# Optimization experiments

Hardware: AMD Instinct MI355X
Metric: run time of the kernel (lower is better)

The kernel has to match this reference:

```python
import jax, jax.numpy as jnp
import numpy as np

B, T, N, H, DH = 32, 64, 100, 4, 32  # batch, seq, nodes, heads, dim/head


def setup_inputs() -> dict:
    key = jax.random.key(0)
    ks = jax.random.split(key, 20)
    # structured flat observation: [action_mask(132), adj(100*100), dt(1), obs(256), siem(128)]
    am = (jax.random.uniform(ks[0], (B, T, 132)) < 0.8).astype(jnp.float32)
    adj = (jax.random.uniform(ks[1], (B, T, N * N)) < 0.05).astype(jnp.float32)
    dt = jax.random.uniform(ks[2], (B, T, 1)) * 0.1 + 0.01
    obs = jax.random.normal(ks[3], (B, T, 256))
    siem = jax.random.normal(ks[4], (B, T, 128))
    inputs = jnp.concatenate([am, adj, dt, obs, siem], axis=-1)
    s = 0.05
    return dict(
        inputs=inputs,
        h0=jnp.zeros((B, 128), jnp.float32),
        fc_w=jax.random.normal(ks[5], (384, 256)) * s,
        fc_b=jnp.zeros((256,)),
        gat_w=jax.random.normal(ks[6], (256, H, DH)) * s,
        a_src=jax.random.normal(ks[7], (H, DH)) * s,
        a_dst=jax.random.normal(ks[8], (H, DH)) * s,
        ode_w1=jax.random.normal(ks[9], (128, 128)) * s,
        ode_b1=jnp.zeros((128,)),
        ode_w2=jax.random.normal(ks[10], (128, 128)) * s,
        ode_b2=jnp.zeros((128,)),
        gru_wi=jax.random.normal(ks[11], (128, 384)) * s,
        gru_wh=jax.random.normal(ks[12], (128, 384)) * s,
        gru_bi=jnp.zeros((384,)),
        gru_bh=jnp.zeros((384,)),
        act_w=jax.random.normal(ks[13], (128, 132)) * s,
        act_b=jnp.zeros((132,)),
        val_w=jax.random.normal(ks[14], (128, 1)) * s,
        val_b=jnp.zeros((1,)),
    )


def reference(inputs, h0, fc_w, fc_b, gat_w, a_src, a_dst, ode_w1, ode_b1,
              ode_w2, ode_b2, gru_wi, gru_wh, gru_bi, gru_bh, act_w, act_b,
              val_w, val_b):
    Bt, Tt = inputs.shape[0], inputs.shape[1]
    action_mask = inputs[..., :132]
    adj_raw = inputs[..., 132:10132].reshape(Bt * Tt, N, N)
    dtn = inputs[..., 10132:10133]                      # [B,T,1]
    x = jnp.concatenate([inputs[..., 10133:10389], inputs[..., 10389:10517]], -1)
    x = jax.nn.relu(x @ fc_w + fc_b).reshape(Bt * Tt, 256)
    # SubnetMaskGenerator.create_mask: binary adjacency + self loops
    adj = (adj_raw > 0) | jnp.eye(N, dtype=bool)[None]
    # place per-agent embedding at node 0, rest zero
    x_nodes = jnp.zeros((Bt * Tt, N, 256), x.dtype).at[:, 0, :].set(x)
    Wh = jnp.einsum('bnf,fhd->bhnd', x_nodes, gat_w)
    src = jnp.einsum('bhnd,hd->bhn', Wh, a_src)
    dst = jnp.einsum('bhnd,hd->bhn', Wh, a_dst)
    e = jax.nn.leaky_relu(src[:, :, :, None] + dst[:, :, None, :], 0.2)
    e = jnp.where(adj[:, None, :, :], e, -1e9)
    alpha = jax.nn.softmax(e, axis=-1)
    hgat = jax.nn.elu(jnp.einsum('bhij,bhjd->bhid', alpha, Wh))
    hgat = hgat.transpose(0, 2, 1, 3).reshape(Bt * Tt, N, H * DH)
    x_gat = hgat.mean(axis=1).reshape(Bt, Tt, 128)

    def f(h):  # ODE dynamics net
        return jnp.tanh(jnp.tanh(h @ ode_w1 + ode_b1) @ ode_w2 + ode_b2)

    def step(h, inp):
        xt, dt = inp                                    # [B,128], [B,1]
        k1 = f(h)
        k2 = f(h + 0.5 * dt * k1)
        k3 = f(h + 0.5 * dt * k2)
        k4 = f(h + dt * k3)
        h_ode = h + dt / 6.0 * (k1 + 2 * k2 + 2 * k3 + k4)
        gi = xt @ gru_wi + gru_bi
        gh = h_ode @ gru_wh + gru_bh
        ir, iz, inn = jnp.split(gi, 3, -1)
        hr, hz, hn = jnp.split(gh, 3, -1)
        r = jax.nn.sigmoid(ir + hr)
        z = jax.nn.sigmoid(iz + hz)
        n = jnp.tanh(inn + r * hn)
        h_new = (1.0 - z) * n + z * h_ode
        return h_new, h_new

    h_T, hs = jax.lax.scan(step, h0, (x_gat.transpose(1, 0, 2), dtn.transpose(1, 0, 2)))
    x_rnn = hs.transpose(1, 0, 2)                       # [B,T,128]
    logits = x_rnn @ act_w + act_b
    value = (x_rnn @ val_w + val_b).reshape(-1)
    masked_logits = jnp.where(action_mask == 0.0, jnp.float32(-1e10), logits)
    return masked_logits, h_T, value
```

## Files before the change

### kernel.cpp

```cpp
#include <hip/hip_runtime.h>

#define NIN 10517
typedef unsigned short ushort_t;
using f32x4  = __attribute__((ext_vector_type(4))) float;
using bf16x8 = __attribute__((ext_vector_type(8))) short;

__device__ __forceinline__ float lrelu02(float x){ return x > 0.f ? x : 0.2f*x; }
__device__ __forceinline__ float fast_tanh(float x){ float e=__expf(2.f*x); return 1.f - 2.f/(e+1.f); }
__device__ __forceinline__ float fast_sig(float x){ return 1.f/(1.f+__expf(-x)); }

__device__ __forceinline__ ushort_t f2bf(float x){
  unsigned u = __float_as_uint(x);
  unsigned r = u + 0x7FFF + ((u >> 16) & 1);
  return (ushort_t)(r >> 16);
}
__device__ __forceinline__ float bf2f(ushort_t v){ return __uint_as_float(((unsigned)v) << 16); }

#define LBAR() do { asm volatile("s_waitcnt lgkmcnt(0)" ::: "memory"); \
                    __builtin_amdgcn_s_barrier(); } while (0)

__global__ __launch_bounds__(256) void k_fc_gat(const float* __restrict__ inputs,
    const float* __restrict__ fc_w, const float* __restrict__ fc_b,
    const float* __restrict__ gat_w, const float* __restrict__ a_src, const float* __restrict__ a_dst,
    const float* __restrict__ ode_w1, const float* __restrict__ ode_w2, const float* __restrict__ gru_wh,
    const float* __restrict__ act_w,
    float* __restrict__ wh0_ws, float* __restrict__ sd_ws,
    ushort_t* __restrict__ w1B, ushort_t* __restrict__ w2B, ushort_t* __restrict__ ghB,
    ushort_t* __restrict__ actB)
{
  __shared__ float xin[8][384];
  __shared__ float xfc[8][256];
  __shared__ float wh[8][128];
  const int tid = threadIdx.x;
  const int bt0 = blockIdx.x * 8;

  for (int p = blockIdx.x * 256 + tid; p < 100352; p += 256*256) {
    if (p < 49152) {
      int m = p >> 7, k = p & 127;
      ghB[p] = f2bf(gru_wh[k*384 + m]);
    } else if (p < 65536) {
      int q = p - 49152, jj = q >> 7, k = q & 127;
      w1B[q] = f2bf(ode_w1[k*128 + jj]);
    } else if (p < 81920) {
      int q = p - 65536, jj = q >> 7, k = q & 127;
      w2B[q] = f2bf(ode_w2[k*128 + jj]);
    } else {
      int q = p - 81920, col = q >> 7, k = q & 127;
      actB[q] = (col < 132) ? f2bf(act_w[k*132 + col]) : (ushort_t)0;
    }
  }

  for (int idx = tid; idx < 8*384; idx += 256) {
    int r = idx / 384, f = idx - r*384;
    xin[r][f] = inputs[(size_t)(bt0+r)*NIN + 10133 + f];
  }
  __syncthreads();
  {
    float acc[8];
    float bj = fc_b[tid];
    #pragma unroll
    for (int r=0;r<8;r++) acc[r] = bj;
    for (int f=0; f<384; f++) {
      float wf = fc_w[f*256 + tid];
      #pragma unroll
      for (int r=0;r<8;r++) acc[r] = fmaf(xin[r][f], wf, acc[r]);
    }
    #pragma unroll
    for (int r=0;r<8;r++) xfc[r][tid] = fmaxf(acc[r], 0.f);
  }
  __syncthreads();
  {
    const int j2 = tid & 127, r0 = (tid >> 7) * 4;
    float acc[4];
    #pragma unroll
    for (int r=0;r<4;r++) acc[r] = 0.f;
    for (int f=0; f<256; f++) {
      float wf = gat_w[f*128 + j2];
      #pragma unroll
      for (int r=0;r<4;r++) acc[r] = fmaf(xfc[r0+r][f], wf, acc[r]);
    }
    #pragma unroll
    for (int r=0;r<4;r++) {
      wh[r0+r][j2] = acc[r];
      wh0_ws[(size_t)(bt0+r0+r)*128 + j2] = acc[r];
    }
  }
  __syncthreads();
  if (tid < 64) {
    const int r = tid >> 3, h = (tid >> 1) & 3, w = tid & 1;
    const float* av = w ? a_dst : a_src;
    float acc = 0.f;
    #pragma unroll
    for (int d=0; d<32; d++) acc = fmaf(wh[r][h*32+d], av[h*32+d], acc);
    sd_ws[(size_t)(bt0+r)*8 + w*4 + h] = acc;
  }
}

__global__ __launch_bounds__(256) void k_alpha_gi(const float* __restrict__ inputs,
    const float* __restrict__ wh0_ws, const float* __restrict__ sd_ws,
    const float* __restrict__ gru_wi, const float* __restrict__ gru_bi,
    float* __restrict__ gi_ws)
{
  __shared__ int cnt[100];
  __shared__ int a0f[100];
  __shared__ float alpha[4][100];
  __shared__ float wh0[128];
  __shared__ float sdl[8];
  __shared__ float xg[128];
  __shared__ float psum[256];
  const int tid = threadIdx.x;
  const size_t bt = blockIdx.x;
  if (tid < 128) wh0[tid] = wh0_ws[bt*128 + tid];
  if (tid < 8) sdl[tid] = sd_ws[bt*8 + tid];
  const float* adj = inputs + bt*NIN + 132;
  const int wv = tid >> 6, lane = tid & 63;
  for (int i = wv; i < 100; i += 4) {
    float v0 = adj[i*100 + lane];
    int pred0 = (lane != 0) && ((v0 > 0.f) || (lane == i));
    unsigned long long b0 = __ballot(pred0);
    int pred1 = 0;
    if (lane < 36) {
      float v1 = adj[i*100 + 64 + lane];
      pred1 = (v1 > 0.f) || ((64 + lane) == i);
    }
    unsigned long long b1 = __ballot(pred1);
    if (lane == 0) {
      cnt[i] = __popcll(b0) + __popcll(b1);
      a0f[i] = (v0 > 0.f) ? 1 : 0;
    }
  }
  __syncthreads();
  for (int idx = tid; idx < 400; idx += 256) {
    int h = idx / 100, i = idx - h*100;
    float s = sdl[h], d = sdl[4+h];
    float a;
    if (i == 0) {
      float ea = __expf(lrelu02(s + d));
      float eb = __expf(lrelu02(s));
      a = ea / (ea + (float)cnt[0] * eb);
    } else if (a0f[i]) {
      float ed = __expf(lrelu02(d));
      a = ed / (ed + (float)cnt[i]);
    } else {
      a = 0.f;
    }
    alpha[h][i] = a;
  }
  __syncthreads();
  {
    const int pr = tid & 127, hf = tid >> 7;
    const float w = wh0[pr];
    const int hh = pr >> 5;
    float sum = 0.f;
    const int i0 = hf * 50;
    for (int i = i0; i < i0 + 50; i++) {
      float t = alpha[hh][i] * w;
      sum += (t > 0.f) ? t : (__expf(t) - 1.f);
    }
    psum[tid] = sum;
  }
  __syncthreads();
  if (tid < 128) xg[tid] = (psum[tid] + psum[tid+128]) * 0.01f;
  __syncthreads();
  for (int jj = tid; jj < 384; jj += 256) {
    float acc = gru_bi[jj];
    for (int f=0; f<128; f++) acc = fmaf(xg[f], gru_wi[f*384 + jj], acc);
    gi_ws[bt*384 + jj] = acc;
  }
}

__global__ __launch_bounds__(512) void k_rnn(const float* __restrict__ inputs,
    const float* __restrict__ h0,
    const ushort_t* __restrict__ w1B, const float* __restrict__ ode_b1,
    const ushort_t* __restrict__ w2B, const float* __restrict__ ode_b2,
    const ushort_t* __restrict__ ghB, const float* __restrict__ gru_bh,
    const ushort_t* __restrict__ actB, const float* __restrict__ act_b,
    const float* __restrict__ val_w, const float* __restrict__ val_b,
    const float* __restrict__ gi_ws,
    float* __restrict__ out_logits, float* __restrict__ out_hT, float* __restrict__ out_val)
{
  __shared__ __align__(16) ushort_t bufA[128];
  __shared__ __align__(16) ushort_t bufB[128];
  __shared__ __align__(16) ushort_t bufC[128];
  __shared__ float dtbuf[64];
  __shared__ __align__(16) ushort_t hsbuf[64*136];
  const int tid = threadIdx.x;
  const int b = blockIdx.x;
  const int w = tid >> 6, lane = tid & 63;
  const int li = lane & 15, g = lane >> 4;
  const int col = w*16 + li;

  bf16x8 W1f[4], W2f[4], GAf[4], GBf[4], GCf[4];
  #pragma unroll
  for (int kt=0;kt<4;kt++){
    const int o = kt*32 + g*8;
    W1f[kt] = *reinterpret_cast<const bf16x8*>(w1B + col*128 + o);
    W2f[kt] = *reinterpret_cast<const bf16x8*>(w2B + col*128 + o);
    GAf[kt] = *reinterpret_cast<const bf16x8*>(ghB + (size_t)col*128       + o);
    GBf[kt] = *reinterpret_cast<const bf16x8*>(ghB + (size_t)(col+128)*128 + o);
    GCf[kt] = *reinterpret_cast<const bf16x8*>(ghB + (size_t)(col+256)*128 + o);
  }
  const float b1 = ode_b1[col], b2 = ode_b2[col];
  const float bh0 = gru_bh[col], bh1 = gru_bh[col+128], bh2 = gru_bh[col+256];
  float h = h0[b*128 + col];
  if (tid < 64) dtbuf[tid] = inputs[((size_t)b*64 + tid)*NIN + 10132];
  if (lane < 16) bufC[col] = f2bf(h);
  const float* gib = gi_ws + (size_t)b*64*384 + col;
  __syncthreads();

  bf16x8 af[4];
  auto ldaf = [&](const ushort_t* __restrict__ hb){
    #pragma unroll
    for (int kt=0;kt<4;kt++) af[kt] = *reinterpret_cast<const bf16x8*>(hb + kt*32 + g*8);
  };
  auto mvac = [&](const bf16x8 (&Wf)[4])->float{
    const f32x4 z0 = {0.f,0.f,0.f,0.f};
    f32x4 c0 = __builtin_amdgcn_mfma_f32_16x16x32_bf16(af[0], Wf[0], z0, 0,0,0);
    f32x4 c1 = __builtin_amdgcn_mfma_f32_16x16x32_bf16(af[1], Wf[1], z0, 0,0,0);
    f32x4 c2 = __builtin_amdgcn_mfma_f32_16x16x32_bf16(af[2], Wf[2], z0, 0,0,0);
    f32x4 c3 = __builtin_amdgcn_mfma_f32_16x16x32_bf16(af[3], Wf[3], z0, 0,0,0);
    return (c0[0]+c1[0]) + (c2[0]+c3[0]);
  };

  for (int t=0; t<64; t++) {
    const float dt = dtbuf[t];
    const float gir = gib[(size_t)t*384];
    const float giz = gib[(size_t)t*384 + 128];
    const float gin = gib[(size_t)t*384 + 256];

    float u, k1, k2, k3, k4;
    ldaf(bufC); u  = fast_tanh(mvac(W1f)+b1); if (lane<16) bufA[col]=f2bf(u);                    LBAR();
    ldaf(bufA); k1 = fast_tanh(mvac(W2f)+b2); if (lane<16) bufB[col]=f2bf(fmaf(0.5f*dt,k1,h));   LBAR();
    ldaf(bufB); u  = fast_tanh(mvac(W1f)+b1); if (lane<16) bufA[col]=f2bf(u);                    LBAR();
    ldaf(bufA); k2 = fast_tanh(mvac(W2f)+b2); if (lane<16) bufB[col]=f2bf(fmaf(0.5f*dt,k2,h));   LBAR();
    ldaf(bufB); u  = fast_tanh(mvac(W1f)+b1); if (lane<16) bufA[col]=f2bf(u);                    LBAR();
    ldaf(bufA); k3 = fast_tanh(mvac(W2f)+b2); if (lane<16) bufB[col]=f2bf(fmaf(dt,k3,h));        LBAR();
    ldaf(bufB); u  = fast_tanh(mvac(W1f)+b1); if (lane<16) bufA[col]=f2bf(u);                    LBAR();
    ldaf(bufA); k4 = fast_tanh(mvac(W2f)+b2);
    const float h_ode = fmaf(dt*(1.f/6.f), (k1 + 2.f*k2) + (2.f*k3 + k4), h);
    if (lane<16) bufB[col] = f2bf(h_ode);                                                        LBAR();

    ldaf(bufB);
    {
      const float r = fast_sig(gir + mvac(GAf) + bh0);
      const float z = fast_sig(giz + mvac(GBf) + bh1);
      const float n = fast_tanh(gin + r*(mvac(GCf) + bh2));
      h = (1.f - z)*n + z*h_ode;
    }
    if (lane < 16) {
      bufC[col] = f2bf(h);
      hsbuf[t*136 + col] = f2bf(h);
    }
    LBAR();
  }

  if (lane < 16) out_hT[b*128 + col] = h;

  {
    const int rt = w & 3, ch = w >> 2;
    const int r0 = rt*16;
    bf16x8 haf[4];
    #pragma unroll
    for (int kt=0;kt<4;kt++)
      haf[kt] = *reinterpret_cast<const bf16x8*>(hsbuf + (r0+li)*136 + kt*32 + g*8);
    const int ct0 = ch ? 5 : 0, ctN = ch ? 9 : 5;
    for (int ct=ct0; ct<ctN; ct++){
      const f32x4 z0 = {0.f,0.f,0.f,0.f};
      f32x4 c0, c1, c2, c3;
      {
        const ushort_t* ab = actB + (size_t)(ct*16+li)*128;
        bf16x8 b0 = *reinterpret_cast<const bf16x8*>(ab + 0*32 + g*8);
        bf16x8 b1f = *reinterpret_cast<const bf16x8*>(ab + 1*32 + g*8);
        bf16x8 b2f = *reinterpret_cast<const bf16x8*>(ab + 2*32 + g*8);
        bf16x8 b3f = *reinterpret_cast<const bf16x8*>(ab + 3*32 + g*8);
        c0 = __builtin_amdgcn_mfma_f32_16x16x32_bf16(haf[0], b0,  z0, 0,0,0);
        c1 = __builtin_amdgcn_mfma_f32_16x16x32_bf16(haf[1], b1f, z0, 0,0,0);
        c2 = __builtin_amdgcn_mfma_f32_16x16x32_bf16(haf[2], b2f, z0, 0,0,0);
        c3 = __builtin_amdgcn_mfma_f32_16x16x32_bf16(haf[3], b3f, z0, 0,0,0);
      }
      const int colL = ct*16 + li;
      if (colL < 132){
        const float ab = act_b[colL];
        #pragma unroll
        for (int reg=0; reg<4; reg++){
          const int r = r0 + g*4 + reg;
          const size_t bt = (size_t)b*64 + r;
          const float mval = inputs[bt*NIN + colL];
          const float v = ((c0[reg]+c1[reg]) + (c2[reg]+c3[reg])) + ab;
          out_logits[bt*132 + colL] = (mval == 0.f) ? -1e10f : v;
        }
      }
    }
  }
  if (tid < 64){
    float acc = val_b[0];
    for (int k=0;k<128;k++) acc = fmaf(bf2f(hsbuf[tid*136 + k]), val_w[k], acc);
    out_val[b*64 + tid] = acc;
  }
}

extern "C" void kernel_launch(void* const* d_in, const int* in_sizes, int n_in,
                              void* d_out, int out_size, void* d_ws, size_t ws_size,
                              hipStream_t stream) {
  (void)in_sizes; (void)n_in; (void)out_size; (void)ws_size;
  const float* inputs = (const float*)d_in[0];
  const float* h0     = (const float*)d_in[1];
  const float* fc_w   = (const float*)d_in[2];
  const float* fc_b   = (const float*)d_in[3];
  const float* gat_w  = (const float*)d_in[4];
  const float* a_src  = (const float*)d_in[5];
  const float* a_dst  = (const float*)d_in[6];
  const float* ode_w1 = (const float*)d_in[7];
  const float* ode_b1 = (const float*)d_in[8];
  const float* ode_w2 = (const float*)d_in[9];
  const float* ode_b2 = (const float*)d_in[10];
  const float* gru_wi = (const float*)d_in[11];
  const float* gru_wh = (const float*)d_in[12];
  const float* gru_bi = (const float*)d_in[13];
  const float* gru_bh = (const float*)d_in[14];
  const float* act_w  = (const float*)d_in[15];
  const float* act_b  = (const float*)d_in[16];
  const float* val_w  = (const float*)d_in[17];
  const float* val_b  = (const float*)d_in[18];

  float* ws   = (float*)d_ws;
  float* wh0  = ws;
  float* sd   = ws + 262144;
  float* gi   = ws + 278528;
  ushort_t* w1B  = (ushort_t*)(ws + 1064960);
  ushort_t* w2B  = (ushort_t*)(ws + 1073152);
  ushort_t* ghB  = (ushort_t*)(ws + 1081344);
  ushort_t* actB = (ushort_t*)(ws + 1105920);

  float* out        = (float*)d_out;
  float* out_logits = out;
  float* out_hT     = out + 270336;
  float* out_val    = out + 274432;

  k_fc_gat  <<<dim3(256),  dim3(256), 0, stream>>>(inputs, fc_w, fc_b, gat_w, a_src, a_dst,
                                                   ode_w1, ode_w2, gru_wh, act_w,
                                                   wh0, sd, w1B, w2B, ghB, actB);
  k_alpha_gi<<<dim3(2048), dim3(256), 0, stream>>>(inputs, wh0, sd, gru_wi, gru_bi, gi);
  k_rnn     <<<dim3(32),   dim3(512), 0, stream>>>(inputs, h0, w1B, ode_b1, w2B, ode_b2,
                                                   ghB, gru_bh, actB, act_b, val_w, val_b,
                                                   gi, out_logits, out_hT, out_val);
}
```

Measured before the change: 223.8 us.

## Move GRU input projection into RNN kernel as bf16 MFMA prologue into LDS

The x_gat @ gru_wi projection leaves the alpha kernel, which previously ran a scalar fp32 loop per row and wrote gi to global memory. The alpha kernel now stores only x_gat in bf16. The RNN kernel computes gi for its whole sequence with MFMA at the start and keeps it in LDS. This removes global gi traffic and the scalar matvec, and lets each timestep read gi from LDS instead of global memory. In exchange it adds 96KB of LDS per block, serial prologue work inside the 32-block RNN kernel, and bf16 rounding of the gi inputs.

```diff
diff --git a/kernel.cpp b/kernel.cpp
--- a/kernel.cpp
+++ b/kernel.cpp
@@ -23,10 +23,10 @@
     const float* __restrict__ fc_w, const float* __restrict__ fc_b,
     const float* __restrict__ gat_w, const float* __restrict__ a_src, const float* __restrict__ a_dst,
     const float* __restrict__ ode_w1, const float* __restrict__ ode_w2, const float* __restrict__ gru_wh,
-    const float* __restrict__ act_w,
+    const float* __restrict__ act_w, const float* __restrict__ gru_wi,
     float* __restrict__ wh0_ws, float* __restrict__ sd_ws,
     ushort_t* __restrict__ w1B, ushort_t* __restrict__ w2B, ushort_t* __restrict__ ghB,
-    ushort_t* __restrict__ actB)
+    ushort_t* __restrict__ actB, ushort_t* __restrict__ wiBt)
 {
   __shared__ float xin[8][384];
   __shared__ float xfc[8][256];
@@ -34,7 +34,7 @@
   const int tid = threadIdx.x;
   const int bt0 = blockIdx.x * 8;
 
-  for (int p = blockIdx.x * 256 + tid; p < 100352; p += 256*256) {
+  for (int p = blockIdx.x * 256 + tid; p < 149504; p += 256*256) {
     if (p < 49152) {
       int m = p >> 7, k = p & 127;
       ghB[p] = f2bf(gru_wh[k*384 + m]);
@@ -44,9 +44,12 @@
     } else if (p < 81920) {
       int q = p - 65536, jj = q >> 7, k = q & 127;
       w2B[q] = f2bf(ode_w2[k*128 + jj]);
-    } else {
+    } else if (p < 100352) {
       int q = p - 81920, col = q >> 7, k = q & 127;
       actB[q] = (col < 132) ? f2bf(act_w[k*132 + col]) : (ushort_t)0;
+    } else {
+      int q = p - 100352, m = q >> 7, f = q & 127;
+      wiBt[q] = f2bf(gru_wi[f*384 + m]);
     }
   }
 
@@ -98,15 +101,13 @@
 
 __global__ __launch_bounds__(256) void k_alpha_gi(const float* __restrict__ inputs,
     const float* __restrict__ wh0_ws, const float* __restrict__ sd_ws,
-    const float* __restrict__ gru_wi, const float* __restrict__ gru_bi,
-    float* __restrict__ gi_ws)
+    ushort_t* __restrict__ xg_bf)
 {
   __shared__ int cnt[100];
   __shared__ int a0f[100];
   __shared__ float alpha[4][100];
   __shared__ float wh0[128];
   __shared__ float sdl[8];
-  __shared__ float xg[128];
   __shared__ float psum[256];
   const int tid = threadIdx.x;
   const size_t bt = blockIdx.x;
@@ -160,13 +161,7 @@
     psum[tid] = sum;
   }
   __syncthreads();
-  if (tid < 128) xg[tid] = (psum[tid] + psum[tid+128]) * 0.01f;
-  __syncthreads();
-  for (int jj = tid; jj < 384; jj += 256) {
-    float acc = gru_bi[jj];
-    for (int f=0; f<128; f++) acc = fmaf(xg[f], gru_wi[f*384 + jj], acc);
-    gi_ws[bt*384 + jj] = acc;
-  }
+  if (tid < 128) xg_bf[bt*128 + tid] = f2bf((psum[tid] + psum[tid+128]) * 0.01f);
 }
 
 __global__ __launch_bounds__(512) void k_rnn(const float* __restrict__ inputs,
@@ -176,9 +171,11 @@
     const ushort_t* __restrict__ ghB, const float* __restrict__ gru_bh,
     const ushort_t* __restrict__ actB, const float* __restrict__ act_b,
     const float* __restrict__ val_w, const float* __restrict__ val_b,
-    const float* __restrict__ gi_ws,
+    const ushort_t* __restrict__ xg_bf, const ushort_t* __restrict__ wiBt,
+    const float* __restrict__ gru_bi,
     float* __restrict__ out_logits, float* __restrict__ out_hT, float* __restrict__ out_val)
 {
+  __shared__ float gi_lds[64*384];
   __shared__ __align__(16) ushort_t bufA[128];
   __shared__ __align__(16) ushort_t bufB[128];
   __shared__ __align__(16) ushort_t bufC[128];
@@ -190,6 +187,43 @@
   const int li = lane & 15, g = lane >> 4;
   const int col = w*16 + li;
 
+  {
+    const int rt = w & 3, ch = w >> 2;
+    bf16x8 haf[4];
+    #pragma unroll
+    for (int kt=0;kt<4;kt++)
+      haf[kt] = *reinterpret_cast<const bf16x8*>(xg_bf + ((size_t)(b*64 + rt*16 + li))*128 + kt*32 + g*8);
+    for (int ct = ch*12; ct < ch*12 + 12; ct++) {
+      const int m = ct*16 + li;
+      const f32x4 z0 = {0.f,0.f,0.f,0.f};
+      const ushort_t* wb = wiBt + (size_t)m*128;
+      bf16x8 b0 = *reinterpret_cast<const bf16x8*>(wb + 0*32 + g*8);
+      bf16x8 b1f = *reinterpret_cast<const bf16x8*>(wb + 1*32 + g*8);
+      bf16x8 b2f = *reinterpret_cast<const bf16x8*>(wb + 2*32 + g*8);
+      bf16x8 b3f = *reinterpret_cast<const bf16x8*>(wb + 3*32 + g*8);
+      f32x4 c0 = __builtin_amdgcn_mfma_f32_16x16x32_bf16(haf[0], b0,  z0, 0,0,0);
+      f32x4 c1 = __builtin_amdgcn_mfma_f32_16x16x32_bf16(haf[1], b1f, z0, 0,0,0);
+      f32x4 c2 = __builtin_amdgcn_mfma_f32_16x16x32_bf16(haf[2], b2f, z0, 0,0,0);
+      f32x4 c3 = __builtin_amdgcn_mfma_f32_16x16x32_bf16(haf[3], b3f, z0, 0,0,0);
+      const float bim = gru_bi[m];
+      #pragma unroll
+      for (int r=0;r<4;r++)
+        gi_lds[(rt*16 + g*4 + r)*384 + m] = ((c0[r]+c1[r]) + (c2[r]+c3[r])) + bim;
+    }
+  }
+
+  const float b1 = ode_b1[col], b2 = ode_b2[col];
+  const float bh0 = gru_bh[col], bh1 = gru_bh[col+128], bh2 = gru_bh[col+256];
+  float h = h0[b*128 + col];
+  if (tid < 64) dtbuf[tid] = inputs[((size_t)b*64 + tid)*NIN + 10132];
+  if (lane < 16) bufC[col] = f2bf(h);
+  __syncthreads();
+
+  bf16x8 af[4];
+  auto ldaf = [&](const ushort_t* __restrict__ hb){
+    #pragma unroll
+    for (int kt=0;kt<4;kt++) af[kt] = *reinterpret_cast<const bf16x8*>(hb + kt*32 + g*8);
+  };
   bf16x8 W1f[4], W2f[4], GAf[4], GBf[4], GCf[4];
   #pragma unroll
   for (int kt=0;kt<4;kt++){
@@ -200,19 +234,6 @@
     GBf[kt] = *reinterpret_cast<const bf16x8*>(ghB + (size_t)(col+128)*128 + o);
     GCf[kt] = *reinterpret_cast<const bf16x8*>(ghB + (size_t)(col+256)*128 + o);
   }
-  const float b1 = ode_b1[col], b2 = ode_b2[col];
-  const float bh0 = gru_bh[col], bh1 = gru_bh[col+128], bh2 = gru_bh[col+256];
-  float h = h0[b*128 + col];
-  if (tid < 64) dtbuf[tid] = inputs[((size_t)b*64 + tid)*NIN + 10132];
-  if (lane < 16) bufC[col] = f2bf(h);
-  const float* gib = gi_ws + (size_t)b*64*384 + col;
-  __syncthreads();
-
-  bf16x8 af[4];
-  auto ldaf = [&](const ushort_t* __restrict__ hb){
-    #pragma unroll
-    for (int kt=0;kt<4;kt++) af[kt] = *reinterpret_cast<const bf16x8*>(hb + kt*32 + g*8);
-  };
   auto mvac = [&](const bf16x8 (&Wf)[4])->float{
     const f32x4 z0 = {0.f,0.f,0.f,0.f};
     f32x4 c0 = __builtin_amdgcn_mfma_f32_16x16x32_bf16(af[0], Wf[0], z0, 0,0,0);
@@ -224,9 +245,9 @@
 
   for (int t=0; t<64; t++) {
     const float dt = dtbuf[t];
-    const float gir = gib[(size_t)t*384];
-    const float giz = gib[(size_t)t*384 + 128];
-    const float gin = gib[(size_t)t*384 + 256];
+    const float gir = gi_lds[t*384 + col];
+    const float giz = gi_lds[t*384 + col + 128];
+    const float gin = gi_lds[t*384 + col + 256];
 
     float u, k1, k2, k3, k4;
     ldaf(bufC); u  = fast_tanh(mvac(W1f)+b1); if (lane<16) bufA[col]=f2bf(u);                    LBAR();
@@ -326,11 +347,12 @@
   float* ws   = (float*)d_ws;
   float* wh0  = ws;
   float* sd   = ws + 262144;
-  float* gi   = ws + 278528;
-  ushort_t* w1B  = (ushort_t*)(ws + 1064960);
-  ushort_t* w2B  = (ushort_t*)(ws + 1073152);
-  ushort_t* ghB  = (ushort_t*)(ws + 1081344);
-  ushort_t* actB = (ushort_t*)(ws + 1105920);
+  ushort_t* xg_bf = (ushort_t*)(ws + 278528);
+  ushort_t* w1B   = (ushort_t*)(ws + 409600);
+  ushort_t* w2B   = (ushort_t*)(ws + 417792);
+  ushort_t* ghB   = (ushort_t*)(ws + 425984);
+  ushort_t* actB  = (ushort_t*)(ws + 450560);
+  ushort_t* wiBt  = (ushort_t*)(ws + 459776);
 
   float* out        = (float*)d_out;
   float* out_logits = out;
@@ -338,10 +360,11 @@
   float* out_val    = out + 274432;
 
   k_fc_gat  <<<dim3(256),  dim3(256), 0, stream>>>(inputs, fc_w, fc_b, gat_w, a_src, a_dst,
-                                                   ode_w1, ode_w2, gru_wh, act_w,
-                                                   wh0, sd, w1B, w2B, ghB, actB);
-  k_alpha_gi<<<dim3(2048), dim3(256), 0, stream>>>(inputs, wh0, sd, gru_wi, gru_bi, gi);
+                                                   ode_w1, ode_w2, gru_wh, act_w, gru_wi,
+                                                   wh0, sd, w1B, w2B, ghB, actB, wiBt);
+  k_alpha_gi<<<dim3(2048), dim3(256), 0, stream>>>(inputs, wh0, sd, xg_bf);
   k_rnn     <<<dim3(32),   dim3(512), 0, stream>>>(inputs, h0, w1B, ode_b1, w2B, ode_b2,
                                                    ghB, gru_bh, actB, act_b, val_w, val_b,
-                                                   gi, out_logits, out_hT, out_val);
-}
+                                                   xg_bf, wiBt, gru_bi,
+                                                   out_logits, out_hT, out_val);
+}
```

Measured after the change: 227.8 us. About the same (+1.8%).
